# Kernel tuning notes

Hardware: AMD Instinct MI355X
Metric: run time of the kernel (lower is better)

The kernel has to match this reference:

```python
import jax, jax.numpy as jnp
import numpy as np

B, I, T, O = 256, 182, 2000, 2


def setup_inputs() -> dict:
    key = jax.random.key(0)
    k1, k2, k3, k4, k5 = jax.random.split(key, 5)
    inputs = jax.random.uniform(k1, (B, I, T), dtype=jnp.float32)  # [batch, input_dim, steps]
    W = jax.random.normal(k2, (O, I), dtype=jnp.float32) / np.sqrt(I)
    b = jax.random.normal(k3, (O,), dtype=jnp.float32) * 0.01
    alpha = jax.random.uniform(k4, (O,), dtype=jnp.float32)  # synaptic decay
    beta = jax.random.uniform(k5, (O,), dtype=jnp.float32)   # membrane decay
    return {"inputs": inputs, "W": W, "b": b, "alpha": alpha, "beta": beta}


def reference(inputs, W, b, alpha, beta):
    # SNN branch of DecoderSVM.forward with bin_width_ms//DT == 1 (record mem every step).
    # snntorch Synaptic (reset_mechanism='none'):
    #   syn_t = clamp(alpha,0,1)*syn_{t-1} + curr_t
    #   mem_t = clamp(beta,0,1)*mem_{t-1} + syn_t
    # Spikes are computed but unused since mem_rec records the membrane voltage.
    a = jnp.clip(alpha, 0.0, 1.0)
    bta = jnp.clip(beta, 0.0, 1.0)
    # Precompute all per-step currents in one GEMM: [T, B, O]
    curr = jnp.einsum('bit,oi->tbo', inputs, W) + b

    def step(carry, c):
        syn, mem = carry
        syn = a * syn + c
        mem = bta * mem + syn
        return (syn, mem), mem

    z = jnp.zeros((inputs.shape[0], W.shape[0]), dtype=inputs.dtype)
    _, mem_rec = jax.lax.scan(step, (z, z), curr)  # [T, B, O]
    return jnp.transpose(mem_rec, (1, 0, 2))  # [B, T, O]
```

## Files before the change

kernel.cpp:

```cpp
#include <hip/hip_runtime.h>
#include <hip/hip_bf16.h>

#define BB 256
#define II 182
#define TT 2000
#define OO 2

__global__ __launch_bounds__(512) void snn_fused_kernel(const float* __restrict__ in,
                                                        const float* __restrict__ W,
                                                        const float* __restrict__ bias,
                                                        const float* __restrict__ alpha,
                                                        const float* __restrict__ beta,
                                                        float* __restrict__ out) {
    __shared__ float w0[II];
    __shared__ float w1[II];
    __shared__ float curr_s[OO][TT];
    __shared__ float mem_s[TT * OO];

    const int b = blockIdx.x;
    const int tid = threadIdx.x;

    if (tid < II) {
        w0[tid] = W[tid];
        w1[tid] = W[II + tid];
    }
    __syncthreads();

    if (tid < TT / 4) {
        const float4* p = (const float4*)(in + (size_t)b * II * TT) + tid;
        float4 a0 = {0.f, 0.f, 0.f, 0.f};
        float4 a1 = {0.f, 0.f, 0.f, 0.f};
#pragma unroll 7
        for (int i = 0; i < II; ++i) {
            const float4 x = p[i * (TT / 4)];
            const float wa = w0[i];
            const float wb = w1[i];
            a0.x += x.x * wa; a0.y += x.y * wa; a0.z += x.z * wa; a0.w += x.w * wa;
            a1.x += x.x * wb; a1.y += x.y * wb; a1.z += x.z * wb; a1.w += x.w * wb;
        }
        const float b0 = bias[0];
        const float b1 = bias[1];
        const int t = tid * 4;
        curr_s[0][t + 0] = a0.x + b0; curr_s[0][t + 1] = a0.y + b0;
        curr_s[0][t + 2] = a0.z + b0; curr_s[0][t + 3] = a0.w + b0;
        curr_s[1][t + 0] = a1.x + b1; curr_s[1][t + 1] = a1.y + b1;
        curr_s[1][t + 2] = a1.z + b1; curr_s[1][t + 3] = a1.w + b1;
    }
    __syncthreads();

    if (tid < OO) {
        const int o = tid;
        const float a  = fminf(fmaxf(alpha[o], 0.f), 1.f);
        const float bt = fminf(fmaxf(beta[o],  0.f), 1.f);
        const float4* c4 = (const float4*)curr_s[o];
        float syn = 0.f, mem = 0.f;
        for (int t4 = 0; t4 < TT / 4; ++t4) {
            const float4 x = c4[t4];
            const int t = t4 * 4;
            syn = a * syn + x.x; mem = bt * mem + syn; mem_s[(t + 0) * OO + o] = mem;
            syn = a * syn + x.y; mem = bt * mem + syn; mem_s[(t + 1) * OO + o] = mem;
            syn = a * syn + x.z; mem = bt * mem + syn; mem_s[(t + 2) * OO + o] = mem;
            syn = a * syn + x.w; mem = bt * mem + syn; mem_s[(t + 3) * OO + o] = mem;
        }
    }
    __syncthreads();

    float4* o4 = (float4*)(out + (size_t)b * TT * OO);
    const float4* m4 = (const float4*)mem_s;
#pragma unroll
    for (int idx = tid; idx < TT * OO / 4; idx += 512) {
        o4[idx] = m4[idx];
    }
}

extern "C" void kernel_launch(void* const* d_in, const int* in_sizes, int n_in,
                              void* d_out, int out_size, void* d_ws, size_t ws_size,
                              hipStream_t stream) {
    const float* inputs = (const float*)d_in[0];
    const float* W      = (const float*)d_in[1];
    const float* bias   = (const float*)d_in[2];
    const float* alpha  = (const float*)d_in[3];
    const float* beta   = (const float*)d_in[4];
    float* out = (float*)d_out;

    snn_fused_kernel<<<BB, 512, 0, stream>>>(inputs, W, bias, alpha, beta, out);
}
```

Measured before the change: 512.7 us.

## Parallelize linear recurrence with wavefront chunked scan and padded shared layout

```diff
diff --git a/kernel.cpp b/kernel.cpp
--- a/kernel.cpp
+++ b/kernel.cpp
@@ -14,8 +14,8 @@
                                                         float* __restrict__ out) {
     __shared__ float w0[II];
     __shared__ float w1[II];
-    __shared__ float curr_s[OO][TT];
-    __shared__ float mem_s[TT * OO];
+    __shared__ float curr_sw[OO][2064];
+    __shared__ float mem_sw[OO][2064];
 
     const int b = blockIdx.x;
     const int tid = threadIdx.x;
@@ -40,36 +40,77 @@
         }
         const float b0 = bias[0];
         const float b1 = bias[1];
-        const int t = tid * 4;
-        curr_s[0][t + 0] = a0.x + b0; curr_s[0][t + 1] = a0.y + b0;
-        curr_s[0][t + 2] = a0.z + b0; curr_s[0][t + 3] = a0.w + b0;
-        curr_s[1][t + 0] = a1.x + b1; curr_s[1][t + 1] = a1.y + b1;
-        curr_s[1][t + 2] = a1.z + b1; curr_s[1][t + 3] = a1.w + b1;
+        const int base = tid * 4 + (tid >> 3);
+        curr_sw[0][base + 0] = a0.x + b0; curr_sw[0][base + 1] = a0.y + b0;
+        curr_sw[0][base + 2] = a0.z + b0; curr_sw[0][base + 3] = a0.w + b0;
+        curr_sw[1][base + 0] = a1.x + b1; curr_sw[1][base + 1] = a1.y + b1;
+        curr_sw[1][base + 2] = a1.z + b1; curr_sw[1][base + 3] = a1.w + b1;
     }
     __syncthreads();
 
-    if (tid < OO) {
-        const int o = tid;
-        const float a  = fminf(fmaxf(alpha[o], 0.f), 1.f);
-        const float bt = fminf(fmaxf(beta[o],  0.f), 1.f);
-        const float4* c4 = (const float4*)curr_s[o];
-        float syn = 0.f, mem = 0.f;
-        for (int t4 = 0; t4 < TT / 4; ++t4) {
-            const float4 x = c4[t4];
-            const int t = t4 * 4;
-            syn = a * syn + x.x; mem = bt * mem + syn; mem_s[(t + 0) * OO + o] = mem;
-            syn = a * syn + x.y; mem = bt * mem + syn; mem_s[(t + 1) * OO + o] = mem;
-            syn = a * syn + x.z; mem = bt * mem + syn; mem_s[(t + 2) * OO + o] = mem;
-            syn = a * syn + x.w; mem = bt * mem + syn; mem_s[(t + 3) * OO + o] = mem;
+    {
+        const int wid = tid >> 6;
+        const int lane = tid & 63;
+        if (wid < OO) {
+            const int o = wid;
+            const float a  = fminf(fmaxf(alpha[o], 0.f), 1.f);
+            const float bt = fminf(fmaxf(beta[o],  0.f), 1.f);
+            const int t0 = lane * 32;
+            const int ib = 33 * lane;
+
+            float A = 1.f, Bb = 1.f, S = 0.f, u = 0.f, v = 0.f;
+#pragma unroll
+            for (int k = 0; k < 32; ++k) {
+                const float c = (t0 + k < TT) ? curr_sw[o][ib + k] : 0.f;
+                A *= a;
+                Bb *= bt;
+                S = bt * S + A;
+                u = a * u + c;
+                v = bt * v + u;
+            }
+
+#pragma unroll
+            for (int d = 1; d < 64; d <<= 1) {
+                const float A1 = __shfl_up(A,  (unsigned)d, 64);
+                const float B1 = __shfl_up(Bb, (unsigned)d, 64);
+                const float S1 = __shfl_up(S,  (unsigned)d, 64);
+                const float u1 = __shfl_up(u,  (unsigned)d, 64);
+                const float v1 = __shfl_up(v,  (unsigned)d, 64);
+                if (lane >= d) {
+                    u  = A * u1 + u;
+                    v  = S * u1 + Bb * v1 + v;
+                    S  = S * A1 + Bb * S1;
+                    A  = A * A1;
+                    Bb = Bb * B1;
+                }
+            }
+
+            float syn = __shfl_up(u, 1u, 64);
+            float mem = __shfl_up(v, 1u, 64);
+            if (lane == 0) { syn = 0.f; mem = 0.f; }
+
+#pragma unroll
+            for (int k = 0; k < 32; ++k) {
+                if (t0 + k < TT) {
+                    const float c = curr_sw[o][ib + k];
+                    syn = a * syn + c;
+                    mem = bt * mem + syn;
+                    mem_sw[o][ib + k] = mem;
+                }
+            }
         }
     }
     __syncthreads();
 
-    float4* o4 = (float4*)(out + (size_t)b * TT * OO);
-    const float4* m4 = (const float4*)mem_s;
-#pragma unroll
-    for (int idx = tid; idx < TT * OO / 4; idx += 512) {
-        o4[idx] = m4[idx];
+    if (tid < TT / 4) {
+        const int base = tid * 4 + (tid >> 3);
+        const float m00 = mem_sw[0][base + 0], m10 = mem_sw[1][base + 0];
+        const float m01 = mem_sw[0][base + 1], m11 = mem_sw[1][base + 1];
+        const float m02 = mem_sw[0][base + 2], m12 = mem_sw[1][base + 2];
+        const float m03 = mem_sw[0][base + 3], m13 = mem_sw[1][base + 3];
+        float4* o4 = (float4*)(out + (size_t)b * TT * OO + (size_t)tid * 8);
+        o4[0] = make_float4(m00, m10, m01, m11);
+        o4[1] = make_float4(m02, m12, m03, m13);
     }
 }
 
```

New measurement: 487.0 us. -5.0%, faster.
